# Performance work log

Measured on AMD Instinct MI355X. Metric: run time of the kernel, lower is better.

## Reference

```python
import jax, jax.numpy as jnp
import numpy as np

B, S, D, H, HID = 64, 1024, 128, 4, 512
HD = D // H  # head dim = 32
EPS = 1e-5


def layer_norm(x, gamma, beta):
    mu = jnp.mean(x, axis=-1, keepdims=True)
    var = jnp.mean(jnp.square(x - mu), axis=-1, keepdims=True)
    return (x - mu) * jax.lax.rsqrt(var + EPS) * gamma + beta


def setup_inputs() -> dict:
    key = jax.random.key(0)
    ks = jax.random.split(key, 16)
    w = lambda k, shp: (jax.random.normal(k, shp, dtype=jnp.float32) * 0.02)
    return {
        "seq": jax.random.normal(ks[0], (B, S, D), dtype=jnp.float32),
        "mask": jnp.ones((B, S, 1), dtype=jnp.float32),
        "Wq": w(ks[1], (D, D)), "bq": jnp.zeros((D,), jnp.float32),
        "Wk": w(ks[2], (D, D)), "bk": jnp.zeros((D,), jnp.float32),
        "Wv": w(ks[3], (D, D)), "bv": jnp.zeros((D,), jnp.float32),
        "g1": jnp.ones((D,), jnp.float32), "be1": jnp.zeros((D,), jnp.float32),
        "g2": jnp.ones((D,), jnp.float32), "be2": jnp.zeros((D,), jnp.float32),
        "W1": w(ks[4], (D, HID)), "bm1": jnp.zeros((HID,), jnp.float32),
        "W2": w(ks[5], (HID, D)), "bm2": jnp.zeros((D,), jnp.float32),
    }


def reference(seq, mask, Wq, bq, Wk, bk, Wv, bv, g1, be1, g2, be2, W1, bm1, W2, bm2):
    # pre-norm queries; keys/values come from the RAW seq (SASRec quirk)
    q_in = layer_norm(seq, g1, be1)           # [B,S,D]
    keys = seq

    Q = (q_in @ Wq + bq).reshape(B, S, H, HD)
    K = (keys @ Wk + bk).reshape(B, S, H, HD)
    V = (keys @ Wv + bv).reshape(B, S, H, HD)

    scores = jnp.einsum("bqhd,bkhd->bhqk", Q, K) / jnp.sqrt(jnp.float32(HD))

    # key padding mask from sign of abs-sum over feature dim
    key_mask = jnp.sign(jnp.sum(jnp.abs(keys), axis=-1))      # [B,S]
    scores = jnp.where(key_mask[:, None, None, :] == 0, -jnp.inf, scores)

    # causal mask
    causal = jnp.tril(jnp.ones((S, S), dtype=bool))
    scores = jnp.where(causal[None, None], scores, -jnp.inf)

    w = jax.nn.softmax(scores, axis=-1)
    w = jnp.nan_to_num(w, nan=0.0, posinf=0.0, neginf=0.0)

    # query padding mask (on the NORMALIZED queries)
    query_mask = jnp.sign(jnp.sum(jnp.abs(q_in), axis=-1))    # [B,S]
    w = w * query_mask[:, None, :, None]
    attentions = w                                            # [B,H,S,S]

    attn_out = jnp.einsum("bhqk,bkhd->bqhd", w, V).reshape(B, S, D)

    x = attn_out + q_in
    x = layer_norm(x, g2, be2)
    h = jax.nn.relu(x @ W1 + bm1)
    y = h @ W2 + bm2 + x
    y = y * mask
    return y, attentions
```

## Files before the change

kernel.cpp:

```cpp
#include <hip/hip_runtime.h>
#include <cstddef>
#include <cstdint>

#define BB 64
#define SS 1024
#define DDIM 128
#define NH 4
#define HDIM 32
#define HIDD 512
#define EPSF 1e-5f
#define SCALEF 0.17677669529663687f
#define LOG2E 1.4426950408889634f

typedef __attribute__((ext_vector_type(8))) short short8;
typedef __attribute__((ext_vector_type(4))) short short4_t;
typedef __attribute__((ext_vector_type(4))) float f32x4;
typedef unsigned short ushort_t;

__device__ __forceinline__ unsigned short f2bf(float f) {
  unsigned u = __builtin_bit_cast(unsigned, f);
  unsigned r = (u + 0x7FFFu + ((u >> 16) & 1u)) >> 16;
  return (unsigned short)r;
}
__device__ __forceinline__ float bf2f(ushort_t h) {
  unsigned u = ((unsigned)h) << 16;
  return __builtin_bit_cast(float, u);
}

__global__ __launch_bounds__(256) void k_cvtw(
    const float* __restrict__ Wq, const float* __restrict__ Wk,
    const float* __restrict__ Wv, const float* __restrict__ W1,
    const float* __restrict__ W2,
    ushort_t* __restrict__ WqT, ushort_t* __restrict__ WkT,
    ushort_t* __restrict__ WvT, ushort_t* __restrict__ W1T,
    ushort_t* __restrict__ W2T) {
  __shared__ float tile[32][33];
  const int bid = blockIdx.x;
  const float* src; ushort_t* dst; int K, N, t0;
  if (bid < 16)       { src = Wq; dst = WqT; K = 128; N = 128; t0 = bid; }
  else if (bid < 32)  { src = Wk; dst = WkT; K = 128; N = 128; t0 = bid - 16; }
  else if (bid < 48)  { src = Wv; dst = WvT; K = 128; N = 128; t0 = bid - 32; }
  else if (bid < 112) { src = W1; dst = W1T; K = 128; N = 512; t0 = bid - 48; }
  else                { src = W2; dst = W2T; K = 512; N = 128; t0 = bid - 112; }
  const int ntile = N >> 5;
  const int k0 = (t0 / ntile) * 32, n0 = (t0 % ntile) * 32;
  const int t = threadIdx.x;
  const int r = t >> 3, c = (t & 7) * 4;
  float4 v = *(const float4*)(src + (size_t)(k0 + r) * N + n0 + c);
  tile[r][c] = v.x; tile[r][c + 1] = v.y; tile[r][c + 2] = v.z; tile[r][c + 3] = v.w;
  __syncthreads();
  ushort4 o;
  o.x = f2bf(tile[c + 0][r]); o.y = f2bf(tile[c + 1][r]);
  o.z = f2bf(tile[c + 2][r]); o.w = f2bf(tile[c + 3][r]);
  *(ushort4*)(dst + (size_t)(n0 + r) * K + k0 + c) = o;
}

__global__ __launch_bounds__(256) void k_ln1_qkv(
    const float* __restrict__ seq,
    const float* __restrict__ g1, const float* __restrict__ be1,
    const ushort_t* __restrict__ WqT, const ushort_t* __restrict__ WkT,
    const ushort_t* __restrict__ WvT,
    const float* __restrict__ bq, const float* __restrict__ bk,
    const float* __restrict__ bv,
    ushort_t* __restrict__ q_in16,
    ushort_t* __restrict__ Qo, ushort_t* __restrict__ Ko,
    ushort_t* __restrict__ Vo,
    float* __restrict__ qmask, float* __restrict__ kmask) {
  __shared__ __align__(16) ushort_t qls[64 * 136];
  __shared__ __align__(16) ushort_t sls[64 * 136];
  const int t = threadIdx.x;
  const int row0 = blockIdx.x * 64;

  {
    const int r = t >> 2, s = t & 3;
    const size_t base = (size_t)(row0 + r) * DDIM + s * 32;
    float v[32];
    float sum = 0.f, asum = 0.f;
    #pragma unroll
    for (int i = 0; i < 8; ++i) {
      const f32x4 x4 = *(const f32x4*)(seq + base + i * 4);
      #pragma unroll
      for (int j = 0; j < 4; ++j) {
        v[i * 4 + j] = x4[j];
        sum += x4[j]; asum += fabsf(x4[j]);
      }
    }
    sum += __shfl_xor(sum, 1); sum += __shfl_xor(sum, 2);
    asum += __shfl_xor(asum, 1); asum += __shfl_xor(asum, 2);
    const float mean = sum * (1.f / DDIM);
    float sq = 0.f;
    #pragma unroll
    for (int i = 0; i < 32; ++i) { const float d = v[i] - mean; sq += d * d; }
    sq += __shfl_xor(sq, 1); sq += __shfl_xor(sq, 2);
    const float rsq = rsqrtf(sq * (1.f / DDIM) + EPSF);
    float aq = 0.f;
    #pragma unroll
    for (int i = 0; i < 8; ++i) {
      const f32x4 g4 = *(const f32x4*)(g1 + s * 32 + i * 4);
      const f32x4 b4 = *(const f32x4*)(be1 + s * 32 + i * 4);
      short4_t q4, s4v;
      #pragma unroll
      for (int j = 0; j < 4; ++j) {
        const float qv = (v[i * 4 + j] - mean) * rsq * g4[j] + b4[j];
        aq += fabsf(qv);
        q4[j] = (short)f2bf(qv);
        s4v[j] = (short)f2bf(v[i * 4 + j]);
      }
      *(short4_t*)(qls + r * 136 + s * 32 + i * 4) = q4;
      *(short4_t*)(sls + r * 136 + s * 32 + i * 4) = s4v;
      *(short4_t*)(q_in16 + base + i * 4) = q4;
    }
    aq += __shfl_xor(aq, 1); aq += __shfl_xor(aq, 2);
    if (s == 0) {
      kmask[row0 + r] = asum > 0.f ? 1.f : 0.f;
      qmask[row0 + r] = aq > 0.f ? 1.f : 0.f;
    }
  }
  __syncthreads();

  const int w = t >> 6, lane = t & 63;
  const int lr = lane & 15, lg = lane >> 4;
  const int rloc = w * 16 + lr;
  short8 qa[4], sa[4];
  #pragma unroll
  for (int s4 = 0; s4 < 4; ++s4) {
    qa[s4] = *(const short8*)(qls + rloc * 136 + s4 * 32 + lg * 8);
    sa[s4] = *(const short8*)(sls + rloc * 136 + s4 * 32 + lg * 8);
  }
  const float qsc = SCALEF * LOG2E;
  #pragma unroll
  for (int nt = 0; nt < 8; ++nt) {
    f32x4 acc = {0.f, 0.f, 0.f, 0.f};
    #pragma unroll
    for (int s4 = 0; s4 < 4; ++s4) {
      short8 b = *(const short8*)(WqT + (size_t)(nt * 16 + lr) * DDIM + s4 * 32 + lg * 8);
      acc = __builtin_amdgcn_mfma_f32_16x16x32_bf16(b, qa[s4], acc, 0, 0, 0);
    }
    const int n0 = nt * 16 + lg * 4;
    const float4 bb4 = *(const float4*)(bq + n0);
    short4_t o4;
    o4[0] = (short)f2bf((acc[0] + bb4.x) * qsc);
    o4[1] = (short)f2bf((acc[1] + bb4.y) * qsc);
    o4[2] = (short)f2bf((acc[2] + bb4.z) * qsc);
    o4[3] = (short)f2bf((acc[3] + bb4.w) * qsc);
    *(short4_t*)(Qo + (size_t)(row0 + rloc) * DDIM + n0) = o4;
  }
  #pragma unroll
  for (int nt = 0; nt < 8; ++nt) {
    f32x4 accK = {0.f, 0.f, 0.f, 0.f}, accV = {0.f, 0.f, 0.f, 0.f};
    #pragma unroll
    for (int s4 = 0; s4 < 4; ++s4) {
      short8 bk8 = *(const short8*)(WkT + (size_t)(nt * 16 + lr) * DDIM + s4 * 32 + lg * 8);
      short8 bv8 = *(const short8*)(WvT + (size_t)(nt * 16 + lr) * DDIM + s4 * 32 + lg * 8);
      accK = __builtin_amdgcn_mfma_f32_16x16x32_bf16(bk8, sa[s4], accK, 0, 0, 0);
      accV = __builtin_amdgcn_mfma_f32_16x16x32_bf16(bv8, sa[s4], accV, 0, 0, 0);
    }
    const int n0 = nt * 16 + lg * 4;
    const float4 bk4 = *(const float4*)(bk + n0);
    const float4 bv4 = *(const float4*)(bv + n0);
    short4_t k4, v4;
    k4[0] = (short)f2bf(accK[0] + bk4.x); v4[0] = (short)f2bf(accV[0] + bv4.x);
    k4[1] = (short)f2bf(accK[1] + bk4.y); v4[1] = (short)f2bf(accV[1] + bv4.y);
    k4[2] = (short)f2bf(accK[2] + bk4.z); v4[2] = (short)f2bf(accV[2] + bv4.z);
    k4[3] = (short)f2bf(accK[3] + bk4.w); v4[3] = (short)f2bf(accV[3] + bv4.w);
    *(short4_t*)(Ko + (size_t)(row0 + rloc) * DDIM + n0) = k4;
    *(short4_t*)(Vo + (size_t)(row0 + rloc) * DDIM + n0) = v4;
  }
}

__global__ __launch_bounds__(256, 4) void k_attn_mfma(
    const ushort_t* __restrict__ Q, const ushort_t* __restrict__ K,
    const ushort_t* __restrict__ V,
    const float* __restrict__ qmask, const float* __restrict__ kmask,
    float* __restrict__ attn, float* __restrict__ xo) {
  __shared__ __align__(16) ushort_t Ks[2][64 * 40];
  __shared__ __align__(16) ushort_t Vts[2][32 * 72];
  __shared__ __align__(16) ushort_t Wb[4][16 * 88];

  const int t = threadIdx.x;
  const int w = t >> 6, lane = t & 63, lr = lane & 15, lg = lane >> 4;
  const int qi = 7 - (int)blockIdx.x;
  const int q0 = qi << 7;
  const int h = blockIdx.y, b = blockIdx.z;
  const int kend = q0 + 128;
  const int nch = kend >> 6;

  const size_t bS = (size_t)b * SS;
  const ushort_t* Qh = Q + bS * DDIM + h * HDIM;
  const ushort_t* Kh = K + bS * DDIM + h * HDIM;
  const ushort_t* Vh = V + bS * DDIM + h * HDIM;
  float* attn_bh = attn + (size_t)(b * NH + h) * ((size_t)SS * SS);

  {
    const int cnt4 = (SS - kend) >> 2;
    const f32x4 z = {0.f, 0.f, 0.f, 0.f};
    for (int r = w; r < 128; r += 4) {
      float* rowp = attn_bh + (size_t)(q0 + r) * SS + kend;
      for (int c = lane; c < cnt4; c += 64)
        __builtin_nontemporal_store(z, (f32x4*)(rowp + (size_t)c * 4));
    }
  }

  const int qrow0 = q0 + w * 16 + lr;
  const int qrow1 = qrow0 + 64;
  const int deadlim = q0 + w * 16 + 15;
  const short8 qf0 = *(const short8*)(Qh + (size_t)qrow0 * DDIM + lg * 8);
  const short8 qf1 = *(const short8*)(Qh + (size_t)qrow1 * DDIM + lg * 8);

  const int skr = t >> 2, skc = (t & 3) * 8;

  float lsum0 = 0.f, lsum1 = 0.f;
  {
    short8 kreg = *(const short8*)(Kh + (size_t)skr * DDIM + skc);
    *(short8*)(Ks[0] + skr * 40 + skc) = kreg;
    __syncthreads();
    for (int c = 0; c < nch; ++c) {
      const int kc = c << 6;
      const int cur = c & 1;
      if (c + 1 < nch)
        kreg = *(const short8*)(Kh + (size_t)(kc + 64 + skr) * DDIM + skc);
      short8 kf[4];
      #pragma unroll
      for (int T = 0; T < 4; ++T)
        kf[T] = *(const short8*)(Ks[cur] + (T * 16 + lr) * 40 + lg * 8);
      float4 km4[4];
      #pragma unroll
      for (int T = 0; T < 4; ++T)
        km4[T] = *(const float4*)(kmask + bS + kc + T * 16 + lg * 4);
      if (kc <= deadlim) {
        f32x4 acc0[4];
        #pragma unroll
        for (int T = 0; T < 4; ++T)
          acc0[T] = __builtin_amdgcn_mfma_f32_16x16x32_bf16(kf[T], qf0,
                                                            (f32x4){0.f, 0.f, 0.f, 0.f}, 0, 0, 0);
        #pragma unroll
        for (int T = 0; T < 4; ++T) {
          const int k0 = kc + T * 16 + lg * 4;
          #pragma unroll
          for (int r = 0; r < 4; ++r) {
            const float kmv = r == 0 ? km4[T].x : (r == 1 ? km4[T].y : (r == 2 ? km4[T].z : km4[T].w));
            const bool dead = (kmv == 0.f) || (k0 + r > qrow0);
            lsum0 += dead ? 0.f : exp2f(acc0[T][r]);
          }
        }
      }
      {
        f32x4 acc1[4];
        #pragma unroll
        for (int T = 0; T < 4; ++T)
          acc1[T] = __builtin_amdgcn_mfma_f32_16x16x32_bf16(kf[T], qf1,
                                                            (f32x4){0.f, 0.f, 0.f, 0.f}, 0, 0, 0);
        #pragma unroll
        for (int T = 0; T < 4; ++T) {
          const int k0 = kc + T * 16 + lg * 4;
          #pragma unroll
          for (int r = 0; r < 4; ++r) {
            const float kmv = r == 0 ? km4[T].x : (r == 1 ? km4[T].y : (r == 2 ? km4[T].z : km4[T].w));
            const bool dead = (kmv == 0.f) || (k0 + r > qrow1);
            lsum1 += dead ? 0.f : exp2f(acc1[T][r]);
          }
        }
      }
      if (c + 1 < nch)
        *(short8*)(Ks[cur ^ 1] + skr * 40 + skc) = kreg;
      __syncthreads();
    }
  }
  float ssum0 = lsum0, ssum1 = lsum1;
  ssum0 += __shfl_xor(ssum0, 16); ssum0 += __shfl_xor(ssum0, 32);
  ssum1 += __shfl_xor(ssum1, 16); ssum1 += __shfl_xor(ssum1, 32);
  const float inv0 = (ssum0 > 0.f) ? qmask[bS + qrow0] / ssum0 : 0.f;
  const float inv1 = (ssum1 > 0.f) ? qmask[bS + qrow1] / ssum1 : 0.f;

  ushort_t* myW = &Wb[w][0];
  f32x4 o0 = {0.f, 0.f, 0.f, 0.f}, o1 = {0.f, 0.f, 0.f, 0.f};
  f32x4 o2 = {0.f, 0.f, 0.f, 0.f}, o3 = {0.f, 0.f, 0.f, 0.f};

  {
    short8 kreg = *(const short8*)(Kh + (size_t)skr * DDIM + skc);
    short8 vreg = *(const short8*)(Vh + (size_t)lane * DDIM + w * 8);
    *(short8*)(Ks[0] + skr * 40 + skc) = kreg;
    #pragma unroll
    for (int j = 0; j < 8; ++j) Vts[0][(w * 8 + j) * 72 + lane] = (ushort_t)vreg[j];
    __syncthreads();
    for (int c = 0; c < nch; ++c) {
      const int kc = c << 6;
      const int cur = c & 1;
      if (c + 1 < nch) {
        kreg = *(const short8*)(Kh + (size_t)(kc + 64 + skr) * DDIM + skc);
        vreg = *(const short8*)(Vh + (size_t)(kc + 64 + lane) * DDIM + w * 8);
      }
      short8 kf[4];
      #pragma unroll
      for (int T = 0; T < 4; ++T)
        kf[T] = *(const short8*)(Ks[cur] + (T * 16 + lr) * 40 + lg * 8);
      float4 km4[4];
      #pragma unroll
      for (int T = 0; T < 4; ++T)
        km4[T] = *(const float4*)(kmask + bS + kc + T * 16 + lg * 4);

      if (kc <= deadlim) {
        f32x4 acc0[4];
        #pragma unroll
        for (int T = 0; T < 4; ++T)
          acc0[T] = __builtin_amdgcn_mfma_f32_16x16x32_bf16(kf[T], qf0,
                                                            (f32x4){0.f, 0.f, 0.f, 0.f}, 0, 0, 0);
        #pragma unroll
        for (int T = 0; T < 4; ++T) {
          const int k0 = kc + T * 16 + lg * 4;
          f32x4 wv4;
          #pragma unroll
          for (int r = 0; r < 4; ++r) {
            const float kmv = r == 0 ? km4[T].x : (r == 1 ? km4[T].y : (r == 2 ? km4[T].z : km4[T].w));
            const bool dead = (kmv == 0.f) || (k0 + r > qrow0);
            wv4[r] = dead ? 0.f : exp2f(acc0[T][r]) * inv0;
          }
          __builtin_nontemporal_store(wv4, (f32x4*)(attn_bh + (size_t)qrow0 * SS + k0));
          short4_t p4;
          p4[0] = (short)f2bf(wv4[0]); p4[1] = (short)f2bf(wv4[1]);
          p4[2] = (short)f2bf(wv4[2]); p4[3] = (short)f2bf(wv4[3]);
          *(short4_t*)(myW + lr * 88 + T * 16 + lg * 4) = p4;
        }
        const short8 af0 = *(const short8*)(myW + lr * 88 + lg * 8);
        const short8 af1 = *(const short8*)(myW + lr * 88 + 32 + lg * 8);
        const short8 vb00 = *(const short8*)(Vts[cur] + (size_t)(lr) * 72 + lg * 8);
        const short8 vb10 = *(const short8*)(Vts[cur] + (size_t)(lr) * 72 + 32 + lg * 8);
        const short8 vb01 = *(const short8*)(Vts[cur] + (size_t)(16 + lr) * 72 + lg * 8);
        const short8 vb11 = *(const short8*)(Vts[cur] + (size_t)(16 + lr) * 72 + 32 + lg * 8);
        o0 = __builtin_amdgcn_mfma_f32_16x16x32_bf16(vb00, af0, o0, 0, 0, 0);
        o0 = __builtin_amdgcn_mfma_f32_16x16x32_bf16(vb10, af1, o0, 0, 0, 0);
        o1 = __builtin_amdgcn_mfma_f32_16x16x32_bf16(vb01, af0, o1, 0, 0, 0);
        o1 = __builtin_amdgcn_mfma_f32_16x16x32_bf16(vb11, af1, o1, 0, 0, 0);
      } else {
        const f32x4 z = {0.f, 0.f, 0.f, 0.f};
        #pragma unroll
        for (int T = 0; T < 4; ++T)
          __builtin_nontemporal_store(z, (f32x4*)(attn_bh + (size_t)qrow0 * SS + kc + T * 16 + lg * 4));
      }

      {
        f32x4 acc1[4];
        #pragma unroll
        for (int T = 0; T < 4; ++T)
          acc1[T] = __builtin_amdgcn_mfma_f32_16x16x32_bf16(kf[T], qf1,
                                                            (f32x4){0.f, 0.f, 0.f, 0.f}, 0, 0, 0);
        #pragma unroll
        for (int T = 0; T < 4; ++T) {
          const int k0 = kc + T * 16 + lg * 4;
          f32x4 wv4;
          #pragma unroll
          for (int r = 0; r < 4; ++r) {
            const float kmv = r == 0 ? km4[T].x : (r == 1 ? km4[T].y : (r == 2 ? km4[T].z : km4[T].w));
            const bool dead = (kmv == 0.f) || (k0 + r > qrow1);
            wv4[r] = dead ? 0.f : exp2f(acc1[T][r]) * inv1;
          }
          __builtin_nontemporal_store(wv4, (f32x4*)(attn_bh + (size_t)qrow1 * SS + k0));
          short4_t p4;
          p4[0] = (short)f2bf(wv4[0]); p4[1] = (short)f2bf(wv4[1]);
          p4[2] = (short)f2bf(wv4[2]); p4[3] = (short)f2bf(wv4[3]);
          *(short4_t*)(myW + lr * 88 + T * 16 + lg * 4) = p4;
        }
        const short8 af0 = *(const short8*)(myW + lr * 88 + lg * 8);
        const short8 af1 = *(const short8*)(myW + lr * 88 + 32 + lg * 8);
        const short8 vb00 = *(const short8*)(Vts[cur] + (size_t)(lr) * 72 + lg * 8);
        const short8 vb10 = *(const short8*)(Vts[cur] + (size_t)(lr) * 72 + 32 + lg * 8);
        const short8 vb01 = *(const short8*)(Vts[cur] + (size_t)(16 + lr) * 72 + lg * 8);
        const short8 vb11 = *(const short8*)(Vts[cur] + (size_t)(16 + lr) * 72 + 32 + lg * 8);
        o2 = __builtin_amdgcn_mfma_f32_16x16x32_bf16(vb00, af0, o2, 0, 0, 0);
        o2 = __builtin_amdgcn_mfma_f32_16x16x32_bf16(vb10, af1, o2, 0, 0, 0);
        o3 = __builtin_amdgcn_mfma_f32_16x16x32_bf16(vb01, af0, o3, 0, 0, 0);
        o3 = __builtin_amdgcn_mfma_f32_16x16x32_bf16(vb11, af1, o3, 0, 0, 0);
      }

      if (c + 1 < nch) {
        *(short8*)(Ks[cur ^ 1] + skr * 40 + skc) = kreg;
        #pragma unroll
        for (int j = 0; j < 8; ++j) Vts[cur ^ 1][(w * 8 + j) * 72 + lane] = (ushort_t)vreg[j];
      }
      __syncthreads();
    }
  }

  {
    float* op0 = xo + (bS + qrow0) * DDIM + h * HDIM;
    *(f32x4*)(op0 + lg * 4) = o0;
    *(f32x4*)(op0 + 16 + lg * 4) = o1;
    float* op1 = xo + (bS + qrow1) * DDIM + h * HDIM;
    *(f32x4*)(op1 + lg * 4) = o2;
    *(f32x4*)(op1 + 16 + lg * 4) = o3;
  }
}

__global__ __launch_bounds__(256) void k_mlp_fused(
    const float* __restrict__ xo, const ushort_t* __restrict__ q_in16,
    const float* __restrict__ g2, const float* __restrict__ be2,
    const ushort_t* __restrict__ W1T, const float* __restrict__ bm1,
    const ushort_t* __restrict__ W2T, const float* __restrict__ bm2,
    const float* __restrict__ mask, float* __restrict__ y) {
  __shared__ __align__(16) ushort_t xls[64 * 136];
  __shared__ __align__(16) ushort_t hs[4][16 * 140];
  const int t = threadIdx.x, w = t >> 6, lane = t & 63;
  const int lr = lane & 15, lg = lane >> 4;
  const int row0 = blockIdx.x * 64;

  {
    const int r = t >> 2, s = t & 3;
    const size_t base = (size_t)(row0 + r) * DDIM + s * 32;
    float v[32];
    float sum = 0.f, sq = 0.f;
    #pragma unroll
    for (int i = 0; i < 4; ++i) {
      const f32x4 x4a = *(const f32x4*)(xo + base + i * 8);
      const f32x4 x4b = *(const f32x4*)(xo + base + i * 8 + 4);
      const short8 q8 = *(const short8*)(q_in16 + base + i * 8);
      #pragma unroll
      for (int j = 0; j < 4; ++j) {
        v[i * 8 + j] = x4a[j] + bf2f((ushort_t)q8[j]);
        v[i * 8 + 4 + j] = x4b[j] + bf2f((ushort_t)q8[4 + j]);
      }
    }
    #pragma unroll
    for (int i = 0; i < 32; ++i) { sum += v[i]; sq += v[i] * v[i]; }
    sum += __shfl_xor(sum, 1); sum += __shfl_xor(sum, 2);
    sq  += __shfl_xor(sq, 1);  sq  += __shfl_xor(sq, 2);
    const float mean = sum * (1.f / DDIM);
    const float var = sq * (1.f / DDIM) - mean * mean;
    const float rsq = rsqrtf(var + EPSF);
    #pragma unroll
    for (int i = 0; i < 8; ++i) {
      const f32x4 g4 = *(const f32x4*)(g2 + s * 32 + i * 4);
      const f32x4 b4 = *(const f32x4*)(be2 + s * 32 + i * 4);
      short4_t o4;
      #pragma unroll
      for (int j = 0; j < 4; ++j)
        o4[j] = (short)f2bf((v[i * 4 + j] - mean) * rsq * g4[j] + b4[j]);
      *(short4_t*)(xls + r * 136 + s * 32 + i * 4) = o4;
    }
  }
  __syncthreads();

  ushort_t* myh = &hs[w][0];
  short8 xa[4];
  #pragma unroll
  for (int s = 0; s < 4; ++s)
    xa[s] = *(const short8*)(xls + (w * 16 + lr) * 136 + s * 32 + lg * 8);

  f32x4 yacc[8];
  #pragma unroll
  for (int i = 0; i < 8; ++i) yacc[i] = (f32x4){0.f, 0.f, 0.f, 0.f};

  for (int c = 0; c < 4; ++c) {
    #pragma unroll
    for (int nt = 0; nt < 8; ++nt) {
      f32x4 acc = {0.f, 0.f, 0.f, 0.f};
      #pragma unroll
      for (int s = 0; s < 4; ++s) {
        short8 b = *(const short8*)(W1T + (size_t)(c * 128 + nt * 16 + lr) * DDIM + s * 32 + lg * 8);
        acc = __builtin_amdgcn_mfma_f32_16x16x32_bf16(b, xa[s], acc, 0, 0, 0);
      }
      const int n0 = nt * 16 + lg * 4;
      const float4 bb4 = *(const float4*)(bm1 + c * 128 + n0);
      short4_t hp;
      hp[0] = (short)f2bf(fmaxf(acc[0] + bb4.x, 0.f));
      hp[1] = (short)f2bf(fmaxf(acc[1] + bb4.y, 0.f));
      hp[2] = (short)f2bf(fmaxf(acc[2] + bb4.z, 0.f));
      hp[3] = (short)f2bf(fmaxf(acc[3] + bb4.w, 0.f));
      *(short4_t*)(myh + lr * 140 + n0) = hp;
    }
    short8 a2[4];
    #pragma unroll
    for (int s = 0; s < 4; ++s)
      a2[s] = *(const short8*)(myh + lr * 140 + s * 32 + lg * 8);
    #pragma unroll
    for (int nt = 0; nt < 8; ++nt) {
      #pragma unroll
      for (int s = 0; s < 4; ++s) {
        short8 b = *(const short8*)(W2T + (size_t)(nt * 16 + lr) * HIDD + c * 128 + s * 32 + lg * 8);
        yacc[nt] = __builtin_amdgcn_mfma_f32_16x16x32_bf16(b, a2[s], yacc[nt], 0, 0, 0);
      }
    }
  }

  const int rr = row0 + w * 16 + lr;
  const float mk = mask[rr];
  #pragma unroll
  for (int nt = 0; nt < 8; ++nt) {
    const int n0 = nt * 16 + lg * 4;
    const float4 bb4 = *(const float4*)(bm2 + n0);
    const ushort4 xv = *(const ushort4*)(xls + (w * 16 + lr) * 136 + n0);
    f32x4 out;
    out[0] = (yacc[nt][0] + bb4.x + bf2f(xv.x)) * mk;
    out[1] = (yacc[nt][1] + bb4.y + bf2f(xv.y)) * mk;
    out[2] = (yacc[nt][2] + bb4.z + bf2f(xv.z)) * mk;
    out[3] = (yacc[nt][3] + bb4.w + bf2f(xv.w)) * mk;
    *(f32x4*)(y + (size_t)rr * DDIM + n0) = out;
  }
}

extern "C" void kernel_launch(void* const* d_in, const int* in_sizes, int n_in,
                              void* d_out, int out_size, void* d_ws, size_t ws_size,
                              hipStream_t stream) {
  const float* seq  = (const float*)d_in[0];
  const float* mask = (const float*)d_in[1];
  const float* Wq = (const float*)d_in[2];
  const float* bq = (const float*)d_in[3];
  const float* Wk = (const float*)d_in[4];
  const float* bk = (const float*)d_in[5];
  const float* Wv = (const float*)d_in[6];
  const float* bv = (const float*)d_in[7];
  const float* g1 = (const float*)d_in[8];
  const float* be1 = (const float*)d_in[9];
  const float* g2 = (const float*)d_in[10];
  const float* be2 = (const float*)d_in[11];
  const float* W1 = (const float*)d_in[12];
  const float* bm1 = (const float*)d_in[13];
  const float* W2 = (const float*)d_in[14];
  const float* bm2 = (const float*)d_in[15];

  float* ws   = (float*)d_ws;
  float* xb   = ws;
  float* qmk  = ws + 8388608;
  float* kmk  = ws + 8454144;
  ushort_t* sbase  = (ushort_t*)(ws + 8519680);
  ushort_t* Qb     = sbase;
  ushort_t* Kb     = sbase + 8388608;
  ushort_t* Vb     = sbase + 16777216;
  ushort_t* q_in16 = sbase + 25165824;
  ushort_t* WqT    = sbase + 33554432;
  ushort_t* WkT    = WqT + 16384;
  ushort_t* WvT    = WkT + 16384;
  ushort_t* W1T    = WvT + 16384;
  ushort_t* W2T    = W1T + 65536;

  float* y    = (float*)d_out;
  float* attn = y + 8388608;

  hipLaunchKernelGGL(k_cvtw, dim3(176), dim3(256), 0, stream,
                     Wq, Wk, Wv, W1, W2, WqT, WkT, WvT, W1T, W2T);
  hipLaunchKernelGGL(k_ln1_qkv, dim3(1024), dim3(256), 0, stream,
                     seq, g1, be1, WqT, WkT, WvT, bq, bk, bv,
                     q_in16, Qb, Kb, Vb, qmk, kmk);
  hipLaunchKernelGGL(k_attn_mfma, dim3(8, NH, BB), dim3(256), 0, stream,
                     Qb, Kb, Vb, qmk, kmk, attn, xb);
  hipLaunchKernelGGL(k_mlp_fused, dim3(1024), dim3(256), 0, stream,
                     xb, q_in16, g2, be2, W1T, bm1, W2T, bm2, mask, y);
}
```

Before: 610.6 us.

## Shrink attention query tile to 64 rows, one 16-row slice per wave

The attention kernel now processes 64 query rows per block instead of 128, so each wave handles one 16-row query slice and the grid doubles to 16 query tiles. This removes the second slice's branching and dead-chunk zero-fill path, cuts registers per thread, and drops the occupancy hint from launch bounds. In exchange, each K/V chunk is loaded into shared memory for half as many queries, which roughly doubles K/V global and LDS traffic per query.

Measured after the change: 588.1 us. -3.7%, faster.

```diff
diff --git a/kernel.cpp b/kernel.cpp
--- a/kernel.cpp
+++ b/kernel.cpp
@@ -168,7 +168,7 @@
   }
 }
 
-__global__ __launch_bounds__(256, 4) void k_attn_mfma(
+__global__ __launch_bounds__(256) void k_attn_mfma(
     const ushort_t* __restrict__ Q, const ushort_t* __restrict__ K,
     const ushort_t* __restrict__ V,
     const float* __restrict__ qmask, const float* __restrict__ kmask,
@@ -179,10 +179,10 @@
 
   const int t = threadIdx.x;
   const int w = t >> 6, lane = t & 63, lr = lane & 15, lg = lane >> 4;
-  const int qi = 7 - (int)blockIdx.x;
-  const int q0 = qi << 7;
+  const int qi = 15 - (int)blockIdx.x;
+  const int q0 = qi << 6;
   const int h = blockIdx.y, b = blockIdx.z;
-  const int kend = q0 + 128;
+  const int kend = q0 + 64;
   const int nch = kend >> 6;
 
   const size_t bS = (size_t)b * SS;
@@ -194,22 +194,19 @@
   {
     const int cnt4 = (SS - kend) >> 2;
     const f32x4 z = {0.f, 0.f, 0.f, 0.f};
-    for (int r = w; r < 128; r += 4) {
+    for (int r = w; r < 64; r += 4) {
       float* rowp = attn_bh + (size_t)(q0 + r) * SS + kend;
       for (int c = lane; c < cnt4; c += 64)
         __builtin_nontemporal_store(z, (f32x4*)(rowp + (size_t)c * 4));
     }
   }
 
-  const int qrow0 = q0 + w * 16 + lr;
-  const int qrow1 = qrow0 + 64;
-  const int deadlim = q0 + w * 16 + 15;
-  const short8 qf0 = *(const short8*)(Qh + (size_t)qrow0 * DDIM + lg * 8);
-  const short8 qf1 = *(const short8*)(Qh + (size_t)qrow1 * DDIM + lg * 8);
+  const int qrow = q0 + w * 16 + lr;
+  const short8 qf = *(const short8*)(Qh + (size_t)qrow * DDIM + lg * 8);
 
   const int skr = t >> 2, skc = (t & 3) * 8;
 
-  float lsum0 = 0.f, lsum1 = 0.f;
+  float lsum = 0.f;
   {
     short8 kreg = *(const short8*)(Kh + (size_t)skr * DDIM + skc);
     *(short8*)(Ks[0] + skr * 40 + skc) = kreg;
@@ -223,42 +220,20 @@
       #pragma unroll
       for (int T = 0; T < 4; ++T)
         kf[T] = *(const short8*)(Ks[cur] + (T * 16 + lr) * 40 + lg * 8);
-      float4 km4[4];
+      f32x4 acc[4];
       #pragma unroll
       for (int T = 0; T < 4; ++T)
-        km4[T] = *(const float4*)(kmask + bS + kc + T * 16 + lg * 4);
-      if (kc <= deadlim) {
-        f32x4 acc0[4];
+        acc[T] = __builtin_amdgcn_mfma_f32_16x16x32_bf16(kf[T], qf,
+                                                         (f32x4){0.f, 0.f, 0.f, 0.f}, 0, 0, 0);
+      #pragma unroll
+      for (int T = 0; T < 4; ++T) {
+        const int k0 = kc + T * 16 + lg * 4;
+        const float4 km4 = *(const float4*)(kmask + bS + k0);
         #pragma unroll
-        for (int T = 0; T < 4; ++T)
-          acc0[T] = __builtin_amdgcn_mfma_f32_16x16x32_bf16(kf[T], qf0,
-                                                            (f32x4){0.f, 0.f, 0.f, 0.f}, 0, 0, 0);
-        #pragma unroll
-        for (int T = 0; T < 4; ++T) {
-          const int k0 = kc + T * 16 + lg * 4;
-          #pragma unroll
-          for (int r = 0; r < 4; ++r) {
-            const float kmv = r == 0 ? km4[T].x : (r == 1 ? km4[T].y : (r == 2 ? km4[T].z : km4[T].w));
-            const bool dead = (kmv == 0.f) || (k0 + r > qrow0);
-            lsum0 += dead ? 0.f : exp2f(acc0[T][r]);
-          }
-        }
-      }
-      {
-        f32x4 acc1[4];
-        #pragma unroll
-        for (int T = 0; T < 4; ++T)
-          acc1[T] = __builtin_amdgcn_mfma_f32_16x16x32_bf16(kf[T], qf1,
-                                                            (f32x4){0.f, 0.f, 0.f, 0.f}, 0, 0, 0);
-        #pragma unroll
-        for (int T = 0; T < 4; ++T) {
-          const int k0 = kc + T * 16 + lg * 4;
-          #pragma unroll
-          for (int r = 0; r < 4; ++r) {
-            const float kmv = r == 0 ? km4[T].x : (r == 1 ? km4[T].y : (r == 2 ? km4[T].z : km4[T].w));
-            const bool dead = (kmv == 0.f) || (k0 + r > qrow1);
-            lsum1 += dead ? 0.f : exp2f(acc1[T][r]);
-          }
+        for (int r = 0; r < 4; ++r) {
+          const float kmv = r == 0 ? km4.x : (r == 1 ? km4.y : (r == 2 ? km4.z : km4.w));
+          const bool dead = (kmv == 0.f) || (k0 + r > qrow);
+          lsum += dead ? 0.f : exp2f(acc[T][r]);
         }
       }
       if (c + 1 < nch)
@@ -266,15 +241,14 @@
       __syncthreads();
     }
   }
-  float ssum0 = lsum0, ssum1 = lsum1;
-  ssum0 += __shfl_xor(ssum0, 16); ssum0 += __shfl_xor(ssum0, 32);
-  ssum1 += __shfl_xor(ssum1, 16); ssum1 += __shfl_xor(ssum1, 32);
-  const float inv0 = (ssum0 > 0.f) ? qmask[bS + qrow0] / ssum0 : 0.f;
-  const float inv1 = (ssum1 > 0.f) ? qmask[bS + qrow1] / ssum1 : 0.f;
+  float ssum = lsum;
+  ssum += __shfl_xor(ssum, 16);
+  ssum += __shfl_xor(ssum, 32);
+  const float qm = qmask[bS + qrow];
+  const float inv = (ssum > 0.f) ? qm / ssum : 0.f;
 
   ushort_t* myW = &Wb[w][0];
   f32x4 o0 = {0.f, 0.f, 0.f, 0.f}, o1 = {0.f, 0.f, 0.f, 0.f};
-  f32x4 o2 = {0.f, 0.f, 0.f, 0.f}, o3 = {0.f, 0.f, 0.f, 0.f};
 
   {
     short8 kreg = *(const short8*)(Kh + (size_t)skr * DDIM + skc);
@@ -294,84 +268,38 @@
       #pragma unroll
       for (int T = 0; T < 4; ++T)
         kf[T] = *(const short8*)(Ks[cur] + (T * 16 + lr) * 40 + lg * 8);
-      float4 km4[4];
+      f32x4 acc[4];
       #pragma unroll
       for (int T = 0; T < 4; ++T)
-        km4[T] = *(const float4*)(kmask + bS + kc + T * 16 + lg * 4);
-
-      if (kc <= deadlim) {
-        f32x4 acc0[4];
+        acc[T] = __builtin_amdgcn_mfma_f32_16x16x32_bf16(kf[T], qf,
+                                                         (f32x4){0.f, 0.f, 0.f, 0.f}, 0, 0, 0);
+      #pragma unroll
+      for (int T = 0; T < 4; ++T) {
+        const int k0 = kc + T * 16 + lg * 4;
+        const float4 km4 = *(const float4*)(kmask + bS + k0);
+        f32x4 wv4;
         #pragma unroll
-        for (int T = 0; T < 4; ++T)
-          acc0[T] = __builtin_amdgcn_mfma_f32_16x16x32_bf16(kf[T], qf0,
-                                                            (f32x4){0.f, 0.f, 0.f, 0.f}, 0, 0, 0);
-        #pragma unroll
-        for (int T = 0; T < 4; ++T) {
-          const int k0 = kc + T * 16 + lg * 4;
-          f32x4 wv4;
-          #pragma unroll
-          for (int r = 0; r < 4; ++r) {
-            const float kmv = r == 0 ? km4[T].x : (r == 1 ? km4[T].y : (r == 2 ? km4[T].z : km4[T].w));
-            const bool dead = (kmv == 0.f) || (k0 + r > qrow0);
-            wv4[r] = dead ? 0.f : exp2f(acc0[T][r]) * inv0;
-          }
-          __builtin_nontemporal_store(wv4, (f32x4*)(attn_bh + (size_t)qrow0 * SS + k0));
-          short4_t p4;
-          p4[0] = (short)f2bf(wv4[0]); p4[1] = (short)f2bf(wv4[1]);
-          p4[2] = (short)f2bf(wv4[2]); p4[3] = (short)f2bf(wv4[3]);
-          *(short4_t*)(myW + lr * 88 + T * 16 + lg * 4) = p4;
+        for (int r = 0; r < 4; ++r) {
+          const float kmv = r == 0 ? km4.x : (r == 1 ? km4.y : (r == 2 ? km4.z : km4.w));
+          const bool dead = (kmv == 0.f) || (k0 + r > qrow);
+          wv4[r] = dead ? 0.f : exp2f(acc[T][r]) * inv;
         }
-        const short8 af0 = *(const short8*)(myW + lr * 88 + lg * 8);
-        const short8 af1 = *(const short8*)(myW + lr * 88 + 32 + lg * 8);
-        const short8 vb00 = *(const short8*)(Vts[cur] + (size_t)(lr) * 72 + lg * 8);
-        const short8 vb10 = *(const short8*)(Vts[cur] + (size_t)(lr) * 72 + 32 + lg * 8);
-        const short8 vb01 = *(const short8*)(Vts[cur] + (size_t)(16 + lr) * 72 + lg * 8);
-        const short8 vb11 = *(const short8*)(Vts[cur] + (size_t)(16 + lr) * 72 + 32 + lg * 8);
-        o0 = __builtin_amdgcn_mfma_f32_16x16x32_bf16(vb00, af0, o0, 0, 0, 0);
-        o0 = __builtin_amdgcn_mfma_f32_16x16x32_bf16(vb10, af1, o0, 0, 0, 0);
-        o1 = __builtin_amdgcn_mfma_f32_16x16x32_bf16(vb01, af0, o1, 0, 0, 0);
-        o1 = __builtin_amdgcn_mfma_f32_16x16x32_bf16(vb11, af1, o1, 0, 0, 0);
-      } else {
-        const f32x4 z = {0.f, 0.f, 0.f, 0.f};
-        #pragma unroll
-        for (int T = 0; T < 4; ++T)
-          __builtin_nontemporal_store(z, (f32x4*)(attn_bh + (size_t)qrow0 * SS + kc + T * 16 + lg * 4));
-      }
-
-      {
-        f32x4 acc1[4];
-        #pragma unroll
-        for (int T = 0; T < 4; ++T)
-          acc1[T] = __builtin_amdgcn_mfma_f32_16x16x32_bf16(kf[T], qf1,
-                                                            (f32x4){0.f, 0.f, 0.f, 0.f}, 0, 0, 0);
-        #pragma unroll
-        for (int T = 0; T < 4; ++T) {
-          const int k0 = kc + T * 16 + lg * 4;
-          f32x4 wv4;
-          #pragma unroll
-          for (int r = 0; r < 4; ++r) {
-            const float kmv = r == 0 ? km4[T].x : (r == 1 ? km4[T].y : (r == 2 ? km4[T].z : km4[T].w));
-            const bool dead = (kmv == 0.f) || (k0 + r > qrow1);
-            wv4[r] = dead ? 0.f : exp2f(acc1[T][r]) * inv1;
-          }
-          __builtin_nontemporal_store(wv4, (f32x4*)(attn_bh + (size_t)qrow1 * SS + k0));
-          short4_t p4;
-          p4[0] = (short)f2bf(wv4[0]); p4[1] = (short)f2bf(wv4[1]);
-          p4[2] = (short)f2bf(wv4[2]); p4[3] = (short)f2bf(wv4[3]);
-          *(short4_t*)(myW + lr * 88 + T * 16 + lg * 4) = p4;
-        }
-        const short8 af0 = *(const short8*)(myW + lr * 88 + lg * 8);
-        const short8 af1 = *(const short8*)(myW + lr * 88 + 32 + lg * 8);
-        const short8 vb00 = *(const short8*)(Vts[cur] + (size_t)(lr) * 72 + lg * 8);
-        const short8 vb10 = *(const short8*)(Vts[cur] + (size_t)(lr) * 72 + 32 + lg * 8);
-        const short8 vb01 = *(const short8*)(Vts[cur] + (size_t)(16 + lr) * 72 + lg * 8);
-        const short8 vb11 = *(const short8*)(Vts[cur] + (size_t)(16 + lr) * 72 + 32 + lg * 8);
-        o2 = __builtin_amdgcn_mfma_f32_16x16x32_bf16(vb00, af0, o2, 0, 0, 0);
-        o2 = __builtin_amdgcn_mfma_f32_16x16x32_bf16(vb10, af1, o2, 0, 0, 0);
-        o3 = __builtin_amdgcn_mfma_f32_16x16x32_bf16(vb01, af0, o3, 0, 0, 0);
-        o3 = __builtin_amdgcn_mfma_f32_16x16x32_bf16(vb11, af1, o3, 0, 0, 0);
-      }
-
+        __builtin_nontemporal_store(wv4, (f32x4*)(attn_bh + (size_t)qrow * SS + k0));
+        short4_t p4;
+        p4[0] = (short)f2bf(wv4[0]); p4[1] = (short)f2bf(wv4[1]);
+        p4[2] = (short)f2bf(wv4[2]); p4[3] = (short)f2bf(wv4[3]);
+        *(short4_t*)(myW + lr * 88 + T * 16 + lg * 4) = p4;
+      }
+      const short8 af0 = *(const short8*)(myW + lr * 88 + lg * 8);
+      const short8 af1 = *(const short8*)(myW + lr * 88 + 32 + lg * 8);
+      const short8 vb00 = *(const short8*)(Vts[cur] + (size_t)(lr) * 72 + lg * 8);
+      const short8 vb10 = *(const short8*)(Vts[cur] + (size_t)(lr) * 72 + 32 + lg * 8);
+      const short8 vb01 = *(const short8*)(Vts[cur] + (size_t)(16 + lr) * 72 + lg * 8);
+      const short8 vb11 = *(const short8*)(Vts[cur] + (size_t)(16 + lr) * 72 + 32 + lg * 8);
+      o0 = __builtin_amdgcn_mfma_f32_16x16x32_bf16(vb00, af0, o0, 0, 0, 0);
+      o0 = __builtin_amdgcn_mfma_f32_16x16x32_bf16(vb10, af1, o0, 0, 0, 0);
+      o1 = __builtin_amdgcn_mfma_f32_16x16x32_bf16(vb01, af0, o1, 0, 0, 0);
+      o1 = __builtin_amdgcn_mfma_f32_16x16x32_bf16(vb11, af1, o1, 0, 0, 0);
       if (c + 1 < nch) {
         *(short8*)(Ks[cur ^ 1] + skr * 40 + skc) = kreg;
         #pragma unroll
@@ -382,12 +310,9 @@
   }
 
   {
-    float* op0 = xo + (bS + qrow0) * DDIM + h * HDIM;
-    *(f32x4*)(op0 + lg * 4) = o0;
-    *(f32x4*)(op0 + 16 + lg * 4) = o1;
-    float* op1 = xo + (bS + qrow1) * DDIM + h * HDIM;
-    *(f32x4*)(op1 + lg * 4) = o2;
-    *(f32x4*)(op1 + 16 + lg * 4) = o3;
+    float* op = xo + (bS + qrow) * DDIM + h * HDIM;
+    *(f32x4*)(op + lg * 4) = o0;
+    *(f32x4*)(op + 16 + lg * 4) = o1;
   }
 }
 
@@ -540,7 +465,7 @@
   hipLaunchKernelGGL(k_ln1_qkv, dim3(1024), dim3(256), 0, stream,
                      seq, g1, be1, WqT, WkT, WvT, bq, bk, bv,
                      q_in16, Qb, Kb, Vb, qmk, kmk);
-  hipLaunchKernelGGL(k_attn_mfma, dim3(8, NH, BB), dim3(256), 0, stream,
+  hipLaunchKernelGGL(k_attn_mfma, dim3(16, NH, BB), dim3(256), 0, stream,
                      Qb, Kb, Vb, qmk, kmk, attn, xb);
   hipLaunchKernelGGL(k_mlp_fused, dim3(1024), dim3(256), 0, stream,
                      xb, q_in16, g2, be2, W1T, bm1, W2T, bm2, mask, y);
```
